# Kernel optimization log

Hardware: AMD Instinct MI355X
Metric: run time of the kernel (lower is better)

Reference implementation:

```python
import jax, jax.numpy as jnp
import numpy as np

# static config (matches init_kwargs / chosen grid)
T, H, W = 8, 32, 32          # video token grid
WT, WH, WW = 4, 8, 8         # swin window
HEADS, HD = 16, 128
DIM = HEADS * HD             # 2048
LT = 256                     # text length
EPS = 1e-6
NT, NH, NW_ = T // WT, H // WH, W // WW
NWIN = NT * NH * NW_
WLEN = WT * WH * WW


def rmsnorm(x, g):
    # x: [..., HD], g: [HD]
    var = jnp.mean(x * x, axis=-1, keepdims=True)
    return x * jax.lax.rsqrt(var + EPS) * g


def setup_inputs() -> dict:
    key = jax.random.key(0)
    ks = jax.random.split(key, 8)
    s = 0.02
    Lv = T * H * W
    return {
        'vid': jax.random.normal(ks[0], (Lv, DIM), jnp.float32),
        'txt': jax.random.normal(ks[1], (LT, DIM), jnp.float32),
        'Wqkv_v': jax.random.normal(ks[2], (DIM, 3 * DIM), jnp.float32) * s,
        'bqkv_v': jnp.zeros((3 * DIM,), jnp.float32),
        'Wqkv_t': jax.random.normal(ks[3], (DIM, 3 * DIM), jnp.float32) * s,
        'bqkv_t': jnp.zeros((3 * DIM,), jnp.float32),
        'Wo_v': jax.random.normal(ks[4], (DIM, DIM), jnp.float32) * s,
        'bo_v': jnp.zeros((DIM,), jnp.float32),
        'Wo_t': jax.random.normal(ks[5], (DIM, DIM), jnp.float32) * s,
        'bo_t': jnp.zeros((DIM,), jnp.float32),
        'gq_v': jnp.ones((HD,), jnp.float32),
        'gk_v': jnp.ones((HD,), jnp.float32),
        'gq_t': jnp.ones((HD,), jnp.float32),
        'gk_t': jnp.ones((HD,), jnp.float32),
    }


def _forward(vid, txt, Wqkv_v, bqkv_v, Wqkv_t, bqkv_t, Wo_v, bo_v, Wo_t, bo_t,
             gq_v, gk_v, gq_t, gk_t):
    # per-modality QKV projections
    vqkv = vid @ Wqkv_v + bqkv_v                      # [Lv, 3*DIM]
    tqkv = txt @ Wqkv_t + bqkv_t                      # [LT, 3*DIM]
    # swin window partition: [T,H,W,C] -> [nWin, WLEN, 3, h, d]
    x = vqkv.reshape(NT, WT, NH, WH, NW_, WW, 3 * DIM)
    x = x.transpose(0, 2, 4, 1, 3, 5, 6).reshape(NWIN, WLEN, 3, HEADS, HD)
    vq, vk, vv = x[:, :, 0], x[:, :, 1], x[:, :, 2]
    t = tqkv.reshape(LT, 3, HEADS, HD)
    tq, tk, tv = t[:, 0], t[:, 1], t[:, 2]
    # QK norm (per-head RMSNorm with affine)
    vq, vk = rmsnorm(vq, gq_v), rmsnorm(vk, gk_v)
    tq, tk = rmsnorm(tq, gq_t), rmsnorm(tk, gk_t)
    # concat full text to every window (repeat_concat_idx)
    bt = lambda a: jnp.broadcast_to(a[None], (NWIN,) + a.shape)
    q = jnp.concatenate([vq, bt(tq)], axis=1)          # [nWin, S, h, d]
    k = jnp.concatenate([vk, bt(tk)], axis=1)
    v = jnp.concatenate([vv, bt(tv)], axis=1)
    # attention within each window (flash-varlen equivalent, equal lengths)
    scale = 1.0 / np.sqrt(HD).astype(np.float32)
    scores = jnp.einsum('nqhd,nkhd->nhqk', q, k) * scale
    p = jax.nn.softmax(scores, axis=-1)
    o = jnp.einsum('nhqk,nkhd->nqhd', p, v)            # [nWin, S, h, d]
    vo = o[:, :WLEN].reshape(NWIN, WLEN, DIM)
    to = o[:, WLEN:].mean(axis=0).reshape(LT, DIM)     # un-repeat text: mean over windows
    # window reverse -> flat [Lv, DIM]
    vo = vo.reshape(NT, NH, NW_, WT, WH, WW, DIM)
    vo = vo.transpose(0, 3, 1, 4, 2, 5, 6).reshape(T * H * W, DIM)
    return (vo @ Wo_v + bo_v, to @ Wo_t + bo_t)


def reference(vid, txt, Wqkv_v, bqkv_v, Wqkv_t, bqkv_t, Wo_v, bo_v, Wo_t, bo_t,
              gq_v, gk_v, gq_t, gk_t):
    return _forward(vid, txt, Wqkv_v, bqkv_v, Wqkv_t, bqkv_t, Wo_v, bo_v,
                    Wo_t, bo_t, gq_v, gk_v, gq_t, gk_t)
```

## Files before the change

kernel.cpp:

```cpp
#include <hip/hip_runtime.h>

typedef unsigned short u16;
typedef unsigned int   u32;
typedef __attribute__((ext_vector_type(8))) short short8;
typedef __attribute__((ext_vector_type(4))) float f32x4;

__device__ __forceinline__ u16 f2bf(float f) {
  union { float f; u32 u; } v; v.f = f;
  u32 r = v.u + 0x7fffu + ((v.u >> 16) & 1u);
  return (u16)(r >> 16);
}
__device__ __forceinline__ float bf2f(u32 bits) {
  union { u32 u; float f; } v; v.u = bits << 16; return v.f;
}
__device__ __forceinline__ void gl_lds16(const u16* g, u16* l) {
  __builtin_amdgcn_global_load_lds(
      (const __attribute__((address_space(1))) void*)g,
      (__attribute__((address_space(3))) void*)l, 16, 0, 0);
}

static constexpr int DIM  = 2048;
static constexpr int NQKV = 6144;

__global__ __launch_bounds__(256) void conv_f32_bf16(const float* __restrict__ in,
                                                     u16* __restrict__ out, int n4) {
  int id = blockIdx.x * 256 + threadIdx.x;
  if (id >= n4) return;
  float4 v = ((const float4*)in)[id];
  u32 lo = (u32)f2bf(v.x) | ((u32)f2bf(v.y) << 16);
  u32 hi = (u32)f2bf(v.z) | ((u32)f2bf(v.w) << 16);
  ((uint2*)out)[id] = make_uint2(lo, hi);
}

__global__ void tconv_kernel(const float* __restrict__ W, u16* __restrict__ Wt, int K, int N) {
  __shared__ float t[32][33];
  int tx = threadIdx.x, ty = threadIdx.y;
  int n0 = blockIdx.x * 32, k0 = blockIdx.y * 32;
  #pragma unroll
  for (int i = 0; i < 4; ++i)
    t[ty + i*8][tx] = W[(size_t)(k0 + ty + i*8) * N + n0 + tx];
  __syncthreads();
  #pragma unroll
  for (int i = 0; i < 4; ++i)
    Wt[(size_t)(n0 + ty + i*8) * K + k0 + tx] = f2bf(t[tx][ty + i*8]);
}

__global__ __launch_bounds__(256) void rms_kernel(u16* __restrict__ x,
                                                  const float* __restrict__ g, int nrows) {
  int w = threadIdx.x >> 6, lane = threadIdx.x & 63;
  int rid = blockIdx.x * 4 + w;
  if (rid >= nrows) return;
  u32* row = (u32*)x + (size_t)rid * 64;
  u32 u = row[lane];
  float f0 = bf2f(u & 0xffffu), f1 = bf2f(u >> 16);
  float s = f0*f0 + f1*f1;
  #pragma unroll
  for (int off = 1; off <= 32; off <<= 1) s += __shfl_xor(s, off);
  float r = rsqrtf(s * (1.0f/128.0f) + 1e-6f);
  float g0 = g[lane*2], g1 = g[lane*2+1];
  row[lane] = (u32)f2bf(f0*r*g0) | ((u32)f2bf(f1*r*g1) << 16);
}

__global__ __launch_bounds__(256)
void vtrans_kernel(const u16* __restrict__ src, u16* __restrict__ dst) {
  __shared__ u16 t[64][130];
  int nh = blockIdx.x, k0 = blockIdx.y * 64;
  const u16* s = src + ((size_t)nh*256 + k0)*128;
  u16* d = dst + (size_t)nh*128*256 + k0;
  int tid = threadIdx.x;
  #pragma unroll
  for (int it = 0; it < 4; ++it) {
    int c = tid + it*256;
    int row = c >> 4, ch = c & 15;
    short8 v = *(const short8*)(s + row*128 + ch*8);
    u32* dst32 = (u32*)&t[row][ch*8];
    const u32* v32 = (const u32*)&v;
    dst32[0] = v32[0]; dst32[1] = v32[1]; dst32[2] = v32[2]; dst32[3] = v32[3];
  }
  __syncthreads();
  #pragma unroll
  for (int it = 0; it < 4; ++it) {
    int c = tid + it*256;
    int dr = c >> 3, kg = c & 7;
    short8 v;
    #pragma unroll
    for (int j = 0; j < 8; ++j) v[j] = (short)t[kg*8+j][dr];
    *(short8*)(d + (size_t)dr*256 + kg*8) = v;
  }
}

template<int EPI>
__global__ __launch_bounds__(512, 2)
void gemm256(const u16* __restrict__ A, const u16* __restrict__ Bt,
             const float* __restrict__ bias,
             u16* __restrict__ o0, u16* __restrict__ o1, u16* __restrict__ o2,
             float* __restrict__ of, int ldo, int M, int N, int K)
{
  __shared__ __align__(16) u16 As[4][256*32];
  __shared__ __align__(16) u16 Bs[4][256*32];
  const int NT = K >> 5;
  int tid = threadIdx.x, lane = tid & 63, w = tid >> 6;
  int l15 = lane & 15, l4 = lane >> 4;
  int wm = w >> 2, wn = w & 3;

  int nbx = gridDim.x;
  int nwg = nbx * gridDim.y;
  int bid = blockIdx.y * nbx + blockIdx.x;
  int cpx = nwg >> 3;
  int swz = (bid & 7) * cpx + (bid >> 3);
  int n0 = (swz % nbx) * 256, m0 = (swz / nbx) * 256;

  int srow = tid >> 2, skc = (tid & 3) ^ ((tid >> 3) & 3);
  const u16* aS = A  + (size_t)(m0 + srow) * K + skc * 8;
  const u16* bS = Bt + (size_t)(n0 + srow) * K + skc * 8;
  const size_t halfStride = 128 * (size_t)K;
  const int ldsBase = w * 512;

  #define STAGE_A(slot, tt, half) \
    gl_lds16(aS + (size_t)(tt)*32 + (half)*halfStride, &As[slot][(half)*4096 + ldsBase])
  #define STAGE_B(slot, tt, half) \
    gl_lds16(bS + (size_t)(tt)*32 + (half)*halfStride, &Bs[slot][(half)*4096 + ldsBase])

  #pragma unroll
  for (int pt = 0; pt < 3; ++pt) {
    STAGE_A(pt, pt, 0); STAGE_A(pt, pt, 1);
    STAGE_B(pt, pt, 0); STAGE_B(pt, pt, 1);
  }

  f32x4 acc[8][4] = {};

  for (int t = 0; t < NT; ++t) {
    if (t < NT - 2)       asm volatile("s_waitcnt vmcnt(8)" ::: "memory");
    else if (t == NT - 2) asm volatile("s_waitcnt vmcnt(4)" ::: "memory");
    else                  asm volatile("s_waitcnt vmcnt(0)" ::: "memory");
    __builtin_amdgcn_s_barrier();
    asm volatile("" ::: "memory");

    const u16* ab = As[t & 3];
    const u16* bb = Bs[t & 3];
    bool st = (t + 3 < NT);
    int slot = (t + 3) & 3;

    short8 bf_[4];
    #pragma unroll
    for (int j = 0; j < 4; ++j) {
      int rb = wn*64 + j*16 + l15;
      bf_[j] = *(const short8*)((const char*)bb + rb*64 + ((l4 ^ ((rb>>1)&3))*16));
    }

    short8 af[4];
    #pragma unroll
    for (int i = 0; i < 4; ++i) {
      int ra = wm*128 + i*16 + l15;
      af[i] = *(const short8*)((const char*)ab + ra*64 + ((l4 ^ ((ra>>1)&3))*16));
    }
    if (st) { STAGE_A(slot, t+3, 0); STAGE_A(slot, t+3, 1); }
    __builtin_amdgcn_s_setprio(1);
    #pragma unroll
    for (int i = 0; i < 4; ++i)
      #pragma unroll
      for (int j = 0; j < 4; ++j)
        acc[i][j] = __builtin_amdgcn_mfma_f32_16x16x32_bf16(af[i], bf_[j], acc[i][j], 0, 0, 0);
    __builtin_amdgcn_s_setprio(0);

    #pragma unroll
    for (int i = 0; i < 4; ++i) {
      int ra = wm*128 + 64 + i*16 + l15;
      af[i] = *(const short8*)((const char*)ab + ra*64 + ((l4 ^ ((ra>>1)&3))*16));
    }
    if (st) { STAGE_B(slot, t+3, 0); STAGE_B(slot, t+3, 1); }
    __builtin_amdgcn_s_setprio(1);
    #pragma unroll
    for (int i = 0; i < 4; ++i)
      #pragma unroll
      for (int j = 0; j < 4; ++j)
        acc[4+i][j] = __builtin_amdgcn_mfma_f32_16x16x32_bf16(af[i], bf_[j], acc[4+i][j], 0, 0, 0);
    __builtin_amdgcn_s_setprio(0);
  }
  #undef STAGE_A
  #undef STAGE_B

  #pragma unroll
  for (int i = 0; i < 8; ++i)
    #pragma unroll
    for (int j = 0; j < 4; ++j)
      #pragma unroll
      for (int r = 0; r < 4; ++r) {
        int m = m0 + wm*128 + i*16 + l4*4 + r;
        int n = n0 + wn*64  + j*16 + l15;
        float v = acc[i][j][r] + bias[n];
        if (EPI == 0) {
          int which = n >> 11, head = (n >> 7) & 15, d = n & 127;
          int t = m >> 10, hh = (m >> 5) & 31, ww = m & 31;
          int win = ((t>>2)<<4) + ((hh>>3)<<2) + (ww>>3);
          int p   = ((t&3)<<6) + ((hh&7)<<3) + (ww&7);
          u16* dst = which == 0 ? o0 : (which == 1 ? o1 : o2);
          dst[((size_t)(win*16 + head)*256 + p)*128 + d] = f2bf(v);
        } else {
          of[(size_t)m * ldo + n] = v;
        }
      }
}

template<int EPI>
__global__ __launch_bounds__(256)
void gemm128(const u16* __restrict__ A, const u16* __restrict__ Bt,
             const float* __restrict__ bias,
             u16* __restrict__ o0, u16* __restrict__ o1, u16* __restrict__ o2,
             float* __restrict__ of, int ldo, int M, int N, int K)
{
  __shared__ __align__(16) u16 As[128*32];
  __shared__ __align__(16) u16 Bs[128*32];
  int tid = threadIdx.x, lane = tid & 63, w = tid >> 6;
  int l15 = lane & 15, l4 = lane >> 4;
  int m0 = blockIdx.y * 128, n0 = blockIdx.x * 128;
  int wr = (w >> 1) * 64, wc = (w & 1) * 64;
  f32x4 acc[4][4] = {};

  int o0b = (w    )*1024 + lane*16;
  int o1b = (w + 4)*1024 + lane*16;
  int r0 = o0b >> 6, c0 = ((o0b >> 4) & 3) ^ ((r0 >> 1) & 3);
  int r1 = o1b >> 6, c1 = ((o1b >> 4) & 3) ^ ((r1 >> 1) & 3);
  const u16* a0 = A  + (size_t)(m0 + r0)*K + c0*8;
  const u16* a1 = A  + (size_t)(m0 + r1)*K + c1*8;
  const u16* b0 = Bt + (size_t)(n0 + r0)*K + c0*8;
  const u16* b1 = Bt + (size_t)(n0 + r1)*K + c1*8;
  u16* dA0 = As + (w    )*512;
  u16* dA1 = As + (w + 4)*512;
  u16* dB0 = Bs + (w    )*512;
  u16* dB1 = Bs + (w + 4)*512;

  for (int k0 = 0; k0 < K; k0 += 32) {
    gl_lds16(a0 + k0, dA0);
    gl_lds16(a1 + k0, dA1);
    gl_lds16(b0 + k0, dB0);
    gl_lds16(b1 + k0, dB1);
    __syncthreads();
    short8 af[4], bfr[4];
    #pragma unroll
    for (int t = 0; t < 4; ++t) {
      int ra = wr + t*16 + l15;
      af[t]  = *(const short8*)((const char*)As + ra*64 + ((l4 ^ ((ra>>1)&3))*16));
      int rb = wc + t*16 + l15;
      bfr[t] = *(const short8*)((const char*)Bs + rb*64 + ((l4 ^ ((rb>>1)&3))*16));
    }
    #pragma unroll
    for (int i = 0; i < 4; ++i)
      #pragma unroll
      for (int j = 0; j < 4; ++j)
        acc[i][j] = __builtin_amdgcn_mfma_f32_16x16x32_bf16(af[i], bfr[j], acc[i][j], 0, 0, 0);
    __syncthreads();
  }

  #pragma unroll
  for (int i = 0; i < 4; ++i)
    #pragma unroll
    for (int j = 0; j < 4; ++j)
      #pragma unroll
      for (int r = 0; r < 4; ++r) {
        int m = m0 + wr + i*16 + l4*4 + r;
        int n = n0 + wc + j*16 + l15;
        float v = acc[i][j][r] + bias[n];
        if (EPI == 1) {
          int which = n >> 11, head = (n >> 7) & 15, d = n & 127;
          u16* dst = which == 0 ? o0 : (which == 1 ? o1 : o2);
          dst[((size_t)head*256 + m)*128 + d] = f2bf(v);
        } else {
          of[(size_t)m * ldo + n] = v;
        }
      }
}

__global__ __launch_bounds__(512, 4)
void attn_kernel(const u16* __restrict__ vq, const u16* __restrict__ vk, const u16* __restrict__ vv,
                 const u16* __restrict__ tq, const u16* __restrict__ tk, const u16* __restrict__ tv,
                 const float* __restrict__ gq_v, const float* __restrict__ gq_t,
                 u16* __restrict__ vo, float* __restrict__ to_acc)
{
  __shared__ __align__(16) u16 Ks[2*64*128];
  __shared__ __align__(16) u16 Vt[2*128*64];
  int tid = threadIdx.x, lane = tid & 63, w = tid >> 6;
  int l15 = lane & 15, l4 = lane >> 4;
  int bid = blockIdx.x;
  int logical = (bid & 7) * 256 + (bid >> 3);
  int nh_ = logical >> 2, qq = logical & 3;
  int h = nh_ & 15;
  int n = nh_ >> 4;
  int qt = qq * 128 + w * 16;

  const u16* Qb; const float* gq;
  if (qt < 256) { Qb = vq + ((size_t)nh_*256 + qt)*128; gq = gq_v; }
  else          { Qb = tq + ((size_t)h  *256 + (qt-256))*128; gq = gq_t; }
  short8 qf[4];
  float qv[4][8];
  float ss = 0.f;
  #pragma unroll
  for (int dt = 0; dt < 4; ++dt) {
    qf[dt] = *(const short8*)(Qb + l15*128 + l4*8 + dt*32);
    #pragma unroll
    for (int j = 0; j < 8; ++j) {
      float f = bf2f((u16)qf[dt][j]);
      qv[dt][j] = f; ss += f*f;
    }
  }
  ss += __shfl_xor(ss, 16); ss += __shfl_xor(ss, 32);
  float rr = rsqrtf(ss * (1.0f/128.0f) + 1e-6f);
  #pragma unroll
  for (int dt = 0; dt < 4; ++dt) {
    float4 g0 = *(const float4*)(gq + l4*8 + dt*32);
    float4 g1 = *(const float4*)(gq + l4*8 + dt*32 + 4);
    qf[dt][0] = (short)f2bf(qv[dt][0]*rr*g0.x); qf[dt][1] = (short)f2bf(qv[dt][1]*rr*g0.y);
    qf[dt][2] = (short)f2bf(qv[dt][2]*rr*g0.z); qf[dt][3] = (short)f2bf(qv[dt][3]*rr*g0.w);
    qf[dt][4] = (short)f2bf(qv[dt][4]*rr*g1.x); qf[dt][5] = (short)f2bf(qv[dt][5]*rr*g1.y);
    qf[dt][6] = (short)f2bf(qv[dt][6]*rr*g1.z); qf[dt][7] = (short)f2bf(qv[dt][7]*rr*g1.w);
  }

  int oK0 = w*1024 + lane*16, oK1 = oK0 + 8192;
  int kr0 = oK0 >> 8, kc0 = ((oK0 >> 4) & 15) ^ (kr0 & 7);
  int kr1 = oK1 >> 8, kc1 = ((oK1 >> 4) & 15) ^ (kr1 & 7);
  int vd0 = oK0 >> 7, vc0 = ((oK0 >> 4) & 7) ^ (vd0 & 7);
  int vd1 = oK1 >> 7, vc1 = ((oK1 >> 4) & 7) ^ (vd1 & 7);

  f32x4 o_[8] = {};
  float m_run[4] = {-1e30f,-1e30f,-1e30f,-1e30f};
  float l_run[4] = {0.f,0.f,0.f,0.f};
  const float scale = 0.08838834764831845f;

  #define STAGE_CHUNK(cc, buf)                                                        \
    {                                                                                 \
      int kb = (cc) * 64;                                                             \
      const u16* Kc; const u16* Vb; int vkb;                                          \
      if (kb < 256) { Kc = vk + ((size_t)nh_*256 + kb)*128;                           \
                      Vb = vv + (size_t)nh_*128*256; vkb = kb; }                      \
      else          { Kc = tk + ((size_t)h*256 + (kb-256))*128;                       \
                      Vb = tv + (size_t)h*128*256; vkb = kb - 256; }                  \
      gl_lds16(Kc + kr0*128 + kc0*8, Ks + (buf)*8192 + w*512);                        \
      gl_lds16(Kc + kr1*128 + kc1*8, Ks + (buf)*8192 + w*512 + 4096);                 \
      gl_lds16(Vb + (size_t)vd0*256 + vkb + vc0*8, Vt + (buf)*8192 + w*512);          \
      gl_lds16(Vb + (size_t)vd1*256 + vkb + vc1*8, Vt + (buf)*8192 + w*512 + 4096);   \
    }

  STAGE_CHUNK(0, 0);

  for (int c = 0; c < 8; ++c) {
    int cur = c & 1;
    __builtin_amdgcn_s_barrier();
    if (c < 7) STAGE_CHUNK(c + 1, cur ^ 1);
    if (c < 7) asm volatile("s_waitcnt vmcnt(4)" ::: "memory");
    else       asm volatile("s_waitcnt vmcnt(0)" ::: "memory");
    __builtin_amdgcn_s_barrier();
    const char* KsB = (const char*)(Ks + cur*8192);
    const char* VtB = (const char*)(Vt + cur*8192);

    f32x4 s4[4];
    __builtin_amdgcn_s_setprio(1);
    #pragma unroll
    for (int kt = 0; kt < 4; ++kt) {
      f32x4 sa = {0.f,0.f,0.f,0.f};
      int key = kt*16 + l15;
      #pragma unroll
      for (int dt = 0; dt < 4; ++dt) {
        int c16b = l4 + dt*4;
        short8 kf = *(const short8*)(KsB + key*256 + (((c16b ^ (key&7)))*16));
        sa = __builtin_amdgcn_mfma_f32_16x16x32_bf16(qf[dt], kf, sa, 0, 0, 0);
      }
      s4[kt] = sa;
    }
    __builtin_amdgcn_s_setprio(0);

    float f_[4];
    #pragma unroll
    for (int r = 0; r < 4; ++r) {
      float mx = fmaxf(fmaxf(s4[0][r], s4[1][r]), fmaxf(s4[2][r], s4[3][r])) * scale;
      #pragma unroll
      for (int off = 1; off <= 8; off <<= 1) mx = fmaxf(mx, __shfl_xor(mx, off));
      float nm = fmaxf(m_run[r], mx);
      f_[r] = __expf(m_run[r] - nm);
      m_run[r] = nm;
    }
    float p[4][4];
    #pragma unroll
    for (int kt = 0; kt < 4; ++kt)
      #pragma unroll
      for (int r = 0; r < 4; ++r)
        p[kt][r] = __expf(s4[kt][r]*scale - m_run[r]);
    #pragma unroll
    for (int r = 0; r < 4; ++r) {
      float sum = p[0][r] + p[1][r] + p[2][r] + p[3][r];
      #pragma unroll
      for (int off = 1; off <= 8; off <<= 1) sum += __shfl_xor(sum, off);
      l_run[r] = l_run[r]*f_[r] + sum;
    }
    #pragma unroll
    for (int dt = 0; dt < 8; ++dt) {
      f32x4 t = o_[dt];
      t[0]*=f_[0]; t[1]*=f_[1]; t[2]*=f_[2]; t[3]*=f_[3];
      o_[dt] = t;
    }

    __builtin_amdgcn_s_barrier();
    u16* pw = Ks + cur*8192 + w*1024;
    #pragma unroll
    for (int kt = 0; kt < 4; ++kt)
      #pragma unroll
      for (int r = 0; r < 4; ++r) {
        int q = l4*4 + r;
        pw[q*64 + (((kt*2 + (l15>>3)) ^ (q&7))<<3) + (l15&7)] = f2bf(p[kt][r]);
      }
    #pragma unroll
    for (int ks = 0; ks < 2; ++ks) {
      short8 pa = *(const short8*)((const char*)pw + l15*128 + (((ks*4 + l4) ^ (l15&7))<<4));
      __builtin_amdgcn_s_setprio(1);
      #pragma unroll
      for (int dt = 0; dt < 8; ++dt) {
        int d = dt*16 + l15;
        short8 vf = *(const short8*)(VtB + d*128 + (((ks*4 + l4) ^ (d&7))<<4));
        o_[dt] = __builtin_amdgcn_mfma_f32_16x16x32_bf16(pa, vf, o_[dt], 0, 0, 0);
      }
      __builtin_amdgcn_s_setprio(0);
    }
  }
  #undef STAGE_CHUNK

  float inv[4];
  #pragma unroll
  for (int r = 0; r < 4; ++r) inv[r] = 1.0f / l_run[r];
  int nt = n >> 4, nh2 = (n >> 2) & 3, nw = n & 3;
  #pragma unroll
  for (int dt = 0; dt < 8; ++dt) {
    int d = dt*16 + l15;
    int col = h*128 + d;
    #pragma unroll
    for (int r = 0; r < 4; ++r) {
      float val = o_[dt][r] * inv[r];
      int q = qt + l4*4 + r;
      if (q < 256) {
        int wt = q >> 6, wh = (q >> 3) & 7, ww = q & 7;
        int rg = ((nt*4 + wt)*32 + (nh2*8 + wh))*32 + (nw*8 + ww);
        vo[(size_t)rg*2048 + col] = f2bf(val);
      } else {
        atomicAdd(to_acc + (size_t)(q - 256)*2048 + col, val * (1.0f/32.0f));
      }
    }
  }
}

extern "C" void kernel_launch(void* const* d_in, const int* in_sizes, int n_in,
                              void* d_out, int out_size, void* d_ws, size_t ws_size,
                              hipStream_t stream) {
  const float* vid    = (const float*)d_in[0];
  const float* txt    = (const float*)d_in[1];
  const float* Wqkv_v = (const float*)d_in[2];
  const float* bqkv_v = (const float*)d_in[3];
  const float* Wqkv_t = (const float*)d_in[4];
  const float* bqkv_t = (const float*)d_in[5];
  const float* Wo_v   = (const float*)d_in[6];
  const float* bo_v   = (const float*)d_in[7];
  const float* Wo_t   = (const float*)d_in[8];
  const float* bo_t   = (const float*)d_in[9];
  const float* gq_v   = (const float*)d_in[10];
  const float* gk_v   = (const float*)d_in[11];
  const float* gq_t   = (const float*)d_in[12];
  const float* gk_t   = (const float*)d_in[13];
  float* out = (float*)d_out;

  char* p = (char*)d_ws;
  u16* vid_bf   = (u16*)p;  p += 8192ull*2048*2;
  u16* txt_bf   = (u16*)p;  p += 256ull*2048*2;
  u16* Wqkv_v_t = (u16*)p;  p += 6144ull*2048*2;
  u16* Wqkv_t_t = (u16*)p;  p += 6144ull*2048*2;
  u16* Wo_v_t   = (u16*)p;  p += 2048ull*2048*2;
  u16* Wo_t_t   = (u16*)p;  p += 2048ull*2048*2;
  u16* vq_w     = (u16*)p;  p += 32ull*16*256*128*2;
  u16* vk_w     = (u16*)p;  p += 32ull*16*256*128*2;
  u16* vv_w     = (u16*)p;  p += 32ull*16*256*128*2;
  u16* tq_w     = (u16*)p;  p += 16ull*256*128*2;
  u16* tk_w     = (u16*)p;  p += 16ull*256*128*2;
  u16* tv_w     = (u16*)p;  p += 16ull*256*128*2;
  u16* vo_pre   = (u16*)p;  p += 8192ull*2048*2;
  float* to_pre = (float*)p; p += 256ull*2048*4;
  u16* to_bf    = (u16*)p;  p += 256ull*2048*2;
  u16* vvT = vid_bf;
  u16* tvT = vid_bf + 512ull*128*256;

  hipMemsetAsync(to_pre, 0, 256ull*2048*4, stream);

  conv_f32_bf16<<<dim3(16384), dim3(256), 0, stream>>>(vid, vid_bf, 8192*2048/4);
  conv_f32_bf16<<<dim3(512),   dim3(256), 0, stream>>>(txt, txt_bf, 256*2048/4);
  tconv_kernel<<<dim3(192,64), dim3(32,8), 0, stream>>>(Wqkv_v, Wqkv_v_t, 2048, 6144);
  tconv_kernel<<<dim3(192,64), dim3(32,8), 0, stream>>>(Wqkv_t, Wqkv_t_t, 2048, 6144);
  tconv_kernel<<<dim3(64,64),  dim3(32,8), 0, stream>>>(Wo_v,   Wo_v_t,   2048, 2048);
  tconv_kernel<<<dim3(64,64),  dim3(32,8), 0, stream>>>(Wo_t,   Wo_t_t,   2048, 2048);

  gemm256<0><<<dim3(24,32), dim3(512), 0, stream>>>(vid_bf, Wqkv_v_t, bqkv_v,
      vq_w, vk_w, vv_w, nullptr, 0, 8192, NQKV, DIM);
  gemm128<1><<<dim3(48,2),  dim3(256), 0, stream>>>(txt_bf, Wqkv_t_t, bqkv_t,
      tq_w, tk_w, tv_w, nullptr, 0, 256, NQKV, DIM);

  vtrans_kernel<<<dim3(512,4), dim3(256), 0, stream>>>(vv_w, vvT);
  vtrans_kernel<<<dim3(16,4),  dim3(256), 0, stream>>>(tv_w, tvT);

  rms_kernel<<<dim3(32768), dim3(256), 0, stream>>>(vk_w, gk_v, 32*16*256);
  rms_kernel<<<dim3(1024),  dim3(256), 0, stream>>>(tk_w, gk_t, 16*256);

  attn_kernel<<<dim3(2048), dim3(512), 0, stream>>>(vq_w, vk_w, vvT, tq_w, tk_w, tvT,
                                                    gq_v, gq_t, vo_pre, to_pre);

  conv_f32_bf16<<<dim3(512), dim3(256), 0, stream>>>(to_pre, to_bf, 256*2048/4);

  gemm256<2><<<dim3(8,32), dim3(512), 0, stream>>>(vo_pre, Wo_v_t, bo_v,
      nullptr, nullptr, nullptr, out, 2048, 8192, 2048, 2048);
  gemm128<2><<<dim3(16,2), dim3(256), 0, stream>>>(to_bf, Wo_t_t, bo_t,
      nullptr, nullptr, nullptr, out + 16777216, 2048, 256, 2048, 2048);
}
```

Measured before the change: 644.3 us.

## Replace text atomics with per-window partials and pipeline the small GEMM

The attention kernel no longer does float atomicAdds for the text rows. Each window writes its bf16 partial output into a scratch buffer that reuses the Wqkv_v_t workspace, and a new reduce kernel averages the 32 windows into bf16. This removes the memset, the atomic contention and the separate conversion pass. The 128-tile GEMM used for the text projections now has a 4-slot LDS pipeline with three stages prefetched, vmcnt-based waits and setprio, which hides load latency. The costs are bf16 rounding of the partials before averaging and more scratch traffic.

```diff
diff --git a/kernel.cpp b/kernel.cpp
--- a/kernel.cpp
+++ b/kernel.cpp
@@ -87,6 +87,23 @@
     for (int j = 0; j < 8; ++j) v[j] = (short)t[kg*8+j][dr];
     *(short8*)(d + (size_t)dr*256 + kg*8) = v;
   }
+}
+
+__global__ __launch_bounds__(256)
+void reduce_txt(const u16* __restrict__ part, u16* __restrict__ to_bf) {
+  int row = blockIdx.x, c8 = threadIdx.x;
+  const u16* p = part + (size_t)row*2048 + c8*8;
+  float s[8] = {};
+  #pragma unroll 4
+  for (int wn = 0; wn < 32; ++wn) {
+    short8 v = *(const short8*)(p + (size_t)wn*256*2048);
+    #pragma unroll
+    for (int j = 0; j < 8; ++j) s[j] += bf2f((u16)v[j]);
+  }
+  short8 o;
+  #pragma unroll
+  for (int j = 0; j < 8; ++j) o[j] = (short)f2bf(s[j] * (1.0f/32.0f));
+  *(short8*)(to_bf + (size_t)row*2048 + c8*8) = o;
 }
 
 template<int EPI>
@@ -203,54 +220,73 @@
 }
 
 template<int EPI>
-__global__ __launch_bounds__(256)
-void gemm128(const u16* __restrict__ A, const u16* __restrict__ Bt,
-             const float* __restrict__ bias,
-             u16* __restrict__ o0, u16* __restrict__ o1, u16* __restrict__ o2,
-             float* __restrict__ of, int ldo, int M, int N, int K)
+__global__ __launch_bounds__(256, 2)
+void gemm128p(const u16* __restrict__ A, const u16* __restrict__ Bt,
+              const float* __restrict__ bias,
+              u16* __restrict__ o0, u16* __restrict__ o1, u16* __restrict__ o2,
+              float* __restrict__ of, int ldo, int M, int N, int K)
 {
-  __shared__ __align__(16) u16 As[128*32];
-  __shared__ __align__(16) u16 Bs[128*32];
+  __shared__ __align__(16) u16 As[4][128*32];
+  __shared__ __align__(16) u16 Bs[4][128*32];
+  const int NT = K >> 5;
   int tid = threadIdx.x, lane = tid & 63, w = tid >> 6;
   int l15 = lane & 15, l4 = lane >> 4;
   int m0 = blockIdx.y * 128, n0 = blockIdx.x * 128;
   int wr = (w >> 1) * 64, wc = (w & 1) * 64;
+
+  int srow = tid >> 2, skc = (tid & 3) ^ ((tid >> 3) & 3);
+  const u16* aS = A  + (size_t)(m0 + srow) * K + skc * 8;
+  const u16* bS = Bt + (size_t)(n0 + srow) * K + skc * 8;
+  const size_t halfStride = 64 * (size_t)K;
+  const int ldsBase = w * 512;
+
+  #define STAGE_A(slot, tt, half) \
+    gl_lds16(aS + (size_t)(tt)*32 + (half)*halfStride, &As[slot][(half)*2048 + ldsBase])
+  #define STAGE_B(slot, tt, half) \
+    gl_lds16(bS + (size_t)(tt)*32 + (half)*halfStride, &Bs[slot][(half)*2048 + ldsBase])
+
+  #pragma unroll
+  for (int pt = 0; pt < 3; ++pt) {
+    STAGE_A(pt, pt, 0); STAGE_A(pt, pt, 1);
+    STAGE_B(pt, pt, 0); STAGE_B(pt, pt, 1);
+  }
+
   f32x4 acc[4][4] = {};
 
-  int o0b = (w    )*1024 + lane*16;
-  int o1b = (w + 4)*1024 + lane*16;
-  int r0 = o0b >> 6, c0 = ((o0b >> 4) & 3) ^ ((r0 >> 1) & 3);
-  int r1 = o1b >> 6, c1 = ((o1b >> 4) & 3) ^ ((r1 >> 1) & 3);
-  const u16* a0 = A  + (size_t)(m0 + r0)*K + c0*8;
-  const u16* a1 = A  + (size_t)(m0 + r1)*K + c1*8;
-  const u16* b0 = Bt + (size_t)(n0 + r0)*K + c0*8;
-  const u16* b1 = Bt + (size_t)(n0 + r1)*K + c1*8;
-  u16* dA0 = As + (w    )*512;
-  u16* dA1 = As + (w + 4)*512;
-  u16* dB0 = Bs + (w    )*512;
-  u16* dB1 = Bs + (w + 4)*512;
-
-  for (int k0 = 0; k0 < K; k0 += 32) {
-    gl_lds16(a0 + k0, dA0);
-    gl_lds16(a1 + k0, dA1);
-    gl_lds16(b0 + k0, dB0);
-    gl_lds16(b1 + k0, dB1);
-    __syncthreads();
+  for (int t = 0; t < NT; ++t) {
+    if (t < NT - 2)       asm volatile("s_waitcnt vmcnt(8)" ::: "memory");
+    else if (t == NT - 2) asm volatile("s_waitcnt vmcnt(4)" ::: "memory");
+    else                  asm volatile("s_waitcnt vmcnt(0)" ::: "memory");
+    __builtin_amdgcn_s_barrier();
+    asm volatile("" ::: "memory");
+
+    const u16* ab = As[t & 3];
+    const u16* bb = Bs[t & 3];
+    bool st = (t + 3 < NT);
+    int slot = (t + 3) & 3;
+
     short8 af[4], bfr[4];
     #pragma unroll
-    for (int t = 0; t < 4; ++t) {
-      int ra = wr + t*16 + l15;
-      af[t]  = *(const short8*)((const char*)As + ra*64 + ((l4 ^ ((ra>>1)&3))*16));
-      int rb = wc + t*16 + l15;
-      bfr[t] = *(const short8*)((const char*)Bs + rb*64 + ((l4 ^ ((rb>>1)&3))*16));
-    }
+    for (int i = 0; i < 4; ++i) {
+      int ra = wr + i*16 + l15;
+      af[i]  = *(const short8*)((const char*)ab + ra*64 + ((l4 ^ ((ra>>1)&3))*16));
+      int rb = wc + i*16 + l15;
+      bfr[i] = *(const short8*)((const char*)bb + rb*64 + ((l4 ^ ((rb>>1)&3))*16));
+    }
+    if (st) {
+      STAGE_A(slot, t+3, 0); STAGE_A(slot, t+3, 1);
+      STAGE_B(slot, t+3, 0); STAGE_B(slot, t+3, 1);
+    }
+    __builtin_amdgcn_s_setprio(1);
     #pragma unroll
     for (int i = 0; i < 4; ++i)
       #pragma unroll
       for (int j = 0; j < 4; ++j)
         acc[i][j] = __builtin_amdgcn_mfma_f32_16x16x32_bf16(af[i], bfr[j], acc[i][j], 0, 0, 0);
-    __syncthreads();
-  }
+    __builtin_amdgcn_s_setprio(0);
+  }
+  #undef STAGE_A
+  #undef STAGE_B
 
   #pragma unroll
   for (int i = 0; i < 4; ++i)
@@ -275,7 +311,7 @@
 void attn_kernel(const u16* __restrict__ vq, const u16* __restrict__ vk, const u16* __restrict__ vv,
                  const u16* __restrict__ tq, const u16* __restrict__ tk, const u16* __restrict__ tv,
                  const float* __restrict__ gq_v, const float* __restrict__ gq_t,
-                 u16* __restrict__ vo, float* __restrict__ to_acc)
+                 u16* __restrict__ vo, u16* __restrict__ to_part)
 {
   __shared__ __align__(16) u16 Ks[2*64*128];
   __shared__ __align__(16) u16 Vt[2*128*64];
@@ -439,7 +475,7 @@
         int rg = ((nt*4 + wt)*32 + (nh2*8 + wh))*32 + (nw*8 + ww);
         vo[(size_t)rg*2048 + col] = f2bf(val);
       } else {
-        atomicAdd(to_acc + (size_t)(q - 256)*2048 + col, val * (1.0f/32.0f));
+        to_part[((size_t)n*256 + (q - 256))*2048 + col] = f2bf(val);
       }
     }
   }
@@ -482,8 +518,8 @@
   u16* to_bf    = (u16*)p;  p += 256ull*2048*2;
   u16* vvT = vid_bf;
   u16* tvT = vid_bf + 512ull*128*256;
-
-  hipMemsetAsync(to_pre, 0, 256ull*2048*4, stream);
+  u16* to_part = Wqkv_v_t;
+  (void)to_pre;
 
   conv_f32_bf16<<<dim3(16384), dim3(256), 0, stream>>>(vid, vid_bf, 8192*2048/4);
   conv_f32_bf16<<<dim3(512),   dim3(256), 0, stream>>>(txt, txt_bf, 256*2048/4);
@@ -494,7 +530,7 @@
 
   gemm256<0><<<dim3(24,32), dim3(512), 0, stream>>>(vid_bf, Wqkv_v_t, bqkv_v,
       vq_w, vk_w, vv_w, nullptr, 0, 8192, NQKV, DIM);
-  gemm128<1><<<dim3(48,2),  dim3(256), 0, stream>>>(txt_bf, Wqkv_t_t, bqkv_t,
+  gemm128p<1><<<dim3(48,2), dim3(256), 0, stream>>>(txt_bf, Wqkv_t_t, bqkv_t,
       tq_w, tk_w, tv_w, nullptr, 0, 256, NQKV, DIM);
 
   vtrans_kernel<<<dim3(512,4), dim3(256), 0, stream>>>(vv_w, vvT);
@@ -504,12 +540,12 @@
   rms_kernel<<<dim3(1024),  dim3(256), 0, stream>>>(tk_w, gk_t, 16*256);
 
   attn_kernel<<<dim3(2048), dim3(512), 0, stream>>>(vq_w, vk_w, vvT, tq_w, tk_w, tvT,
-                                                    gq_v, gq_t, vo_pre, to_pre);
-
-  conv_f32_bf16<<<dim3(512), dim3(256), 0, stream>>>(to_pre, to_bf, 256*2048/4);
+                                                    gq_v, gq_t, vo_pre, to_part);
+
+  reduce_txt<<<dim3(256), dim3(256), 0, stream>>>(to_part, to_bf);
 
   gemm256<2><<<dim3(8,32), dim3(512), 0, stream>>>(vo_pre, Wo_v_t, bo_v,
       nullptr, nullptr, nullptr, out, 2048, 8192, 2048, 2048);
-  gemm128<2><<<dim3(16,2), dim3(256), 0, stream>>>(to_bf, Wo_t_t, bo_t,
+  gemm128p<2><<<dim3(16,2), dim3(256), 0, stream>>>(to_bf, Wo_t_t, bo_t,
       nullptr, nullptr, nullptr, out + 16777216, 2048, 256, 2048, 2048);
 }
```

Result: faster. 608.2 us (-5.6%).
